# Performance work log

Measured on AMD Instinct MI355X. Metric: run time of the kernel, lower is better.

Reference implementation:

```python
import jax, jax.numpy as jnp
import numpy as np

B, IN, OUT, FAN = 2048, 4096, 4096, 64

def setup_inputs() -> dict:
    key = jax.random.key(0)
    k1, k2, k3, k4 = jax.random.split(key, 4)
    input = jax.random.normal(k1, (B, IN), dtype=jnp.float32)
    condensed_weight = jax.random.normal(k2, (OUT, FAN), dtype=jnp.float32) * 0.05
    bias = jax.random.normal(k3, (OUT,), dtype=jnp.float32) * 0.05
    input_mask = jax.random.randint(k4, (OUT, FAN), 0, IN, dtype=jnp.int64)
    return {"input": input, "condensed_weight": condensed_weight,
            "bias": bias, "input_mask": input_mask}

def reference(input, condensed_weight, bias, input_mask):
    # Per output neuron o: sum_f input[b, idx[o,f]] * w[o,f] + bias[o]
    # gathered: [B, OUT, FAN] -- the structured-sparse gather
    gathered = jnp.take(input, input_mask, axis=1)
    return jnp.einsum("bof,of->bo", gathered, condensed_weight) + bias
```

## Files before the change

### kernel.cpp

```cpp
#include <hip/hip_runtime.h>

#define B_DIM   2048
#define IN_DIM  4096
#define OUT_DIM 4096
#define FAN     64


typedef float v2f __attribute__((ext_vector_type(2)));

__device__ __forceinline__ unsigned bf16_rne(float f) {
    unsigned u = __float_as_uint(f);
    return (u + 0x7fffu + ((u >> 16) & 1u)) >> 16;
}

__global__ __launch_bounds__(256) void pack_kernel(
    const float* __restrict__ input, uint4* __restrict__ wsp)
{
    const int idx = blockIdx.x * 256 + threadIdx.x;
    const int t   = idx >> 11;
    const int c0  = (idx & 2047) << 1;

    const float* p = input + (size_t)t * 4 * IN_DIM + c0;
    const float2 r0 = *reinterpret_cast<const float2*>(p + 0 * IN_DIM);
    const float2 r1 = *reinterpret_cast<const float2*>(p + 1 * IN_DIM);
    const float2 r2 = *reinterpret_cast<const float2*>(p + 2 * IN_DIM);
    const float2 r3 = *reinterpret_cast<const float2*>(p + 3 * IN_DIM);

    uint4 q;
    q.x = bf16_rne(r0.x) | (bf16_rne(r1.x) << 16);
    q.y = bf16_rne(r2.x) | (bf16_rne(r3.x) << 16);
    q.z = bf16_rne(r0.y) | (bf16_rne(r1.y) << 16);
    q.w = bf16_rne(r2.y) | (bf16_rne(r3.y) << 16);

    wsp[(size_t)t * 2048 + (c0 >> 1)] = q;
}

__global__ __launch_bounds__(256, 2) void condensed_kernel(
    const uint4* __restrict__ wsp,
    const float* __restrict__ weight,
    const float* __restrict__ bias,
    const int*   __restrict__ mask,
    float*       __restrict__ out)
{
    __shared__ __align__(16) uint4 lds[2048];

    const int tid     = threadIdx.x;
    const int o       = blockIdx.y * 256 + tid;
    const int tbase   = blockIdx.x * 8;
    const int rowbase = blockIdx.x * 32;

    unsigned addrs[FAN];
    float    wv[FAN];
    {
        const int4*   mv = reinterpret_cast<const int4*>(mask)     + o * (FAN / 4);
        const float4* wp = reinterpret_cast<const float4*>(weight) + o * (FAN / 4);
        #pragma unroll
        for (int j = 0; j < FAN / 4; ++j) {
            int4   m4 = mv[j];
            float4 w4 = wp[j];
            addrs[4*j+0] = (unsigned)m4.x << 3;
            addrs[4*j+1] = (unsigned)m4.y << 3;
            addrs[4*j+2] = (unsigned)m4.z << 3;
            addrs[4*j+3] = (unsigned)m4.w << 3;
            wv[4*j+0] = w4.x;
            wv[4*j+1] = w4.y;
            wv[4*j+2] = w4.z;
            wv[4*j+3] = w4.w;
        }
    }
    const float bv = bias[o];

    const char* ldsb = reinterpret_cast<const char*>(lds);

    for (int t = 0; t < 8; ++t) {
        if (t) __syncthreads();

        {
            const uint4* src = wsp + (size_t)(tbase + t) * 2048 + tid;
            #pragma unroll
            for (int it = 0; it < 8; ++it) {
                __builtin_amdgcn_global_load_lds(
                    (const __attribute__((address_space(1))) unsigned*)(src + it * 256),
                    (__attribute__((address_space(3))) unsigned*)(lds + it * 256 + tid),
                    16, 0, 0);
            }
        }
        __syncthreads();

        {
            v2f a01 = {0.f, 0.f}, a23 = {0.f, 0.f};
            #pragma unroll
            for (int j = 0; j < FAN; ++j) {
                const uint2 g = *reinterpret_cast<const uint2*>(ldsb + addrs[j]);
                const v2f w2 = {wv[j], wv[j]};
                v2f v;
                v.x = __uint_as_float(g.x << 16);
                v.y = __uint_as_float(g.x & 0xffff0000u);
                a01 = __builtin_elementwise_fma(v, w2, a01);
                v.x = __uint_as_float(g.y << 16);
                v.y = __uint_as_float(g.y & 0xffff0000u);
                a23 = __builtin_elementwise_fma(v, w2, a23);
            }
            float* op = out + (size_t)(rowbase + 4 * t) * OUT_DIM + o;
            op[0 * OUT_DIM] = a01.x + bv;
            op[1 * OUT_DIM] = a01.y + bv;
            op[2 * OUT_DIM] = a23.x + bv;
            op[3 * OUT_DIM] = a23.y + bv;
        }
    }
}

extern "C" void kernel_launch(void* const* d_in, const int* in_sizes, int n_in,
                              void* d_out, int out_size, void* d_ws, size_t ws_size,
                              hipStream_t stream) {
    const float* input  = (const float*)d_in[0];
    const float* weight = (const float*)d_in[1];
    const float* bias   = (const float*)d_in[2];
    const int*   mask   = (const int*)d_in[3];
    float*       out    = (float*)d_out;
    uint4*       wsp    = (uint4*)d_ws;

    pack_kernel<<<4096, 256, 0, stream>>>(input, wsp);
    dim3 grid(64, 16);
    condensed_kernel<<<grid, 256, 0, stream>>>(wsp, weight, bias, mask, out);
}
```

Baseline: 134.7 us.

## Fuse bf16 pack into gather kernel with double-buffered LDS tiles

Drops the separate pack kernel. The gather kernel now loads fp32 input rows itself, converts them to bf16 in registers, and writes them into double-buffered LDS with a new swizzled layout. Blocks grow to 512 threads, with two threads per output neuron each taking half of an 8-row tile, over 128 rows per block, and the next tile's global loads overlap the current gather. This removes the workspace round trip and a launch, but leaves only 256 blocks at one block per CU, uses 128KB of LDS and much higher register pressure.

New measurement: 296.7 us. +120.3%, slower.

```diff
diff --git a/kernel.cpp b/kernel.cpp
--- a/kernel.cpp
+++ b/kernel.cpp
@@ -13,55 +13,87 @@
     return (u + 0x7fffu + ((u >> 16) & 1u)) >> 16;
 }
 
-__global__ __launch_bounds__(256) void pack_kernel(
-    const float* __restrict__ input, uint4* __restrict__ wsp)
-{
-    const int idx = blockIdx.x * 256 + threadIdx.x;
-    const int t   = idx >> 11;
-    const int c0  = (idx & 2047) << 1;
-
-    const float* p = input + (size_t)t * 4 * IN_DIM + c0;
-    const float2 r0 = *reinterpret_cast<const float2*>(p + 0 * IN_DIM);
-    const float2 r1 = *reinterpret_cast<const float2*>(p + 1 * IN_DIM);
-    const float2 r2 = *reinterpret_cast<const float2*>(p + 2 * IN_DIM);
-    const float2 r3 = *reinterpret_cast<const float2*>(p + 3 * IN_DIM);
-
-    uint4 q;
-    q.x = bf16_rne(r0.x) | (bf16_rne(r1.x) << 16);
-    q.y = bf16_rne(r2.x) | (bf16_rne(r3.x) << 16);
-    q.z = bf16_rne(r0.y) | (bf16_rne(r1.y) << 16);
-    q.w = bf16_rne(r2.y) | (bf16_rne(r3.y) << 16);
-
-    wsp[(size_t)t * 2048 + (c0 >> 1)] = q;
+__device__ __forceinline__ float f4e(const float4& v, int i) {
+    return reinterpret_cast<const float*>(&v)[i];
 }
 
-__global__ __launch_bounds__(256, 2) void condensed_kernel(
-    const uint4* __restrict__ wsp,
+#define LOADT(t)                                                              \
+    {                                                                         \
+        const float* s0 = input + (size_t)(rowbase + 8 * (t)) * IN_DIM + (tid << 2); \
+        _Pragma("unroll")                                                     \
+        for (int r = 0; r < 8; ++r) {                                         \
+            st[r]     = *reinterpret_cast<const float4*>(s0 + (size_t)r * IN_DIM);        \
+            st[8 + r] = *reinterpret_cast<const float4*>(s0 + (size_t)r * IN_DIM + 2048); \
+        }                                                                     \
+    }
+
+#define CWRITE(BUF)                                                           \
+    {                                                                         \
+        _Pragma("unroll")                                                     \
+        for (int k = 0; k < 2; ++k) {                                         \
+            _Pragma("unroll")                                                 \
+            for (int i = 0; i < 4; ++i) {                                     \
+                uint4 q;                                                      \
+                q.x = bf16_rne(f4e(st[8*k+0], i)) | (bf16_rne(f4e(st[8*k+1], i)) << 16); \
+                q.y = bf16_rne(f4e(st[8*k+2], i)) | (bf16_rne(f4e(st[8*k+3], i)) << 16); \
+                q.z = bf16_rne(f4e(st[8*k+4], i)) | (bf16_rne(f4e(st[8*k+5], i)) << 16); \
+                q.w = bf16_rne(f4e(st[8*k+6], i)) | (bf16_rne(f4e(st[8*k+7], i)) << 16); \
+                *reinterpret_cast<uint4*>(ldsw + (BUF) + k * 32768             \
+                    + ((tid >> 3) << 9) + (i << 7) + ((tid & 7) << 4)) = q;    \
+            }                                                                 \
+        }                                                                     \
+    }
+
+#define GATHER(BUF, t)                                                        \
+    {                                                                         \
+        v2f a01 = {0.f, 0.f}, a23 = {0.f, 0.f};                               \
+        _Pragma("unroll")                                                     \
+        for (int j = 0; j < FAN; ++j) {                                       \
+            const uint2 g = *reinterpret_cast<const uint2*>(ldsb + (BUF) + addrs[j]); \
+            const v2f w2 = {wv[j], wv[j]};                                    \
+            v2f v;                                                            \
+            v.x = __uint_as_float(g.x << 16);                                 \
+            v.y = __uint_as_float(g.x & 0xffff0000u);                         \
+            a01 = __builtin_elementwise_fma(v, w2, a01);                      \
+            v.x = __uint_as_float(g.y << 16);                                 \
+            v.y = __uint_as_float(g.y & 0xffff0000u);                         \
+            a23 = __builtin_elementwise_fma(v, w2, a23);                      \
+        }                                                                     \
+        float* op = out + (size_t)(rowbase + 8 * (t) + ((tid & 1) << 2)) * OUT_DIM + o; \
+        op[0 * OUT_DIM] = a01.x + bv;                                         \
+        op[1 * OUT_DIM] = a01.y + bv;                                         \
+        op[2 * OUT_DIM] = a23.x + bv;                                         \
+        op[3 * OUT_DIM] = a23.y + bv;                                         \
+    }
+
+__global__ __launch_bounds__(512, 1) void fused_kernel(
+    const float* __restrict__ input,
     const float* __restrict__ weight,
     const float* __restrict__ bias,
     const int*   __restrict__ mask,
     float*       __restrict__ out)
 {
-    __shared__ __align__(16) uint4 lds[2048];
+    __shared__ __align__(16) uint4 lds[8192];
 
     const int tid     = threadIdx.x;
-    const int o       = blockIdx.y * 256 + tid;
-    const int tbase   = blockIdx.x * 8;
-    const int rowbase = blockIdx.x * 32;
+    const int o       = blockIdx.y * 256 + (tid >> 1);
+    const int rowbase = blockIdx.x * 128;
 
     unsigned addrs[FAN];
     float    wv[FAN];
     {
         const int4*   mv = reinterpret_cast<const int4*>(mask)     + o * (FAN / 4);
         const float4* wp = reinterpret_cast<const float4*>(weight) + o * (FAN / 4);
+        const unsigned hoff = (unsigned)(tid & 1) << 3;
         #pragma unroll
         for (int j = 0; j < FAN / 4; ++j) {
             int4   m4 = mv[j];
             float4 w4 = wp[j];
-            addrs[4*j+0] = (unsigned)m4.x << 3;
-            addrs[4*j+1] = (unsigned)m4.y << 3;
-            addrs[4*j+2] = (unsigned)m4.z << 3;
-            addrs[4*j+3] = (unsigned)m4.w << 3;
+            int id;
+            id = m4.x; addrs[4*j+0] = (((unsigned)id >> 5) << 9) | (((unsigned)id & 3) << 7) | ((((unsigned)id >> 2) & 7) << 4) | hoff;
+            id = m4.y; addrs[4*j+1] = (((unsigned)id >> 5) << 9) | (((unsigned)id & 3) << 7) | ((((unsigned)id >> 2) & 7) << 4) | hoff;
+            id = m4.z; addrs[4*j+2] = (((unsigned)id >> 5) << 9) | (((unsigned)id & 3) << 7) | ((((unsigned)id >> 2) & 7) << 4) | hoff;
+            id = m4.w; addrs[4*j+3] = (((unsigned)id >> 5) << 9) | (((unsigned)id & 3) << 7) | ((((unsigned)id >> 2) & 7) << 4) | hoff;
             wv[4*j+0] = w4.x;
             wv[4*j+1] = w4.y;
             wv[4*j+2] = w4.z;
@@ -71,42 +103,27 @@
     const float bv = bias[o];
 
     const char* ldsb = reinterpret_cast<const char*>(lds);
+    char*       ldsw = reinterpret_cast<char*>(lds);
+    float4 st[16];
 
-    for (int t = 0; t < 8; ++t) {
-        if (t) __syncthreads();
+    LOADT(0);
+    CWRITE(0);
+    __syncthreads();
 
-        {
-            const uint4* src = wsp + (size_t)(tbase + t) * 2048 + tid;
-            #pragma unroll
-            for (int it = 0; it < 8; ++it) {
-                __builtin_amdgcn_global_load_lds(
-                    (const __attribute__((address_space(1))) unsigned*)(src + it * 256),
-                    (__attribute__((address_space(3))) unsigned*)(lds + it * 256 + tid),
-                    16, 0, 0);
-            }
+    for (int hp = 0; hp < 8; ++hp) {
+        LOADT(2 * hp + 1);
+        GATHER(0, 2 * hp);
+        CWRITE(65536);
+        __syncthreads();
+
+        if (hp < 7) {
+            LOADT(2 * hp + 2);
+            GATHER(65536, 2 * hp + 1);
+            CWRITE(0);
+        } else {
+            GATHER(65536, 2 * hp + 1);
         }
         __syncthreads();
-
-        {
-            v2f a01 = {0.f, 0.f}, a23 = {0.f, 0.f};
-            #pragma unroll
-            for (int j = 0; j < FAN; ++j) {
-                const uint2 g = *reinterpret_cast<const uint2*>(ldsb + addrs[j]);
-                const v2f w2 = {wv[j], wv[j]};
-                v2f v;
-                v.x = __uint_as_float(g.x << 16);
-                v.y = __uint_as_float(g.x & 0xffff0000u);
-                a01 = __builtin_elementwise_fma(v, w2, a01);
-                v.x = __uint_as_float(g.y << 16);
-                v.y = __uint_as_float(g.y & 0xffff0000u);
-                a23 = __builtin_elementwise_fma(v, w2, a23);
-            }
-            float* op = out + (size_t)(rowbase + 4 * t) * OUT_DIM + o;
-            op[0 * OUT_DIM] = a01.x + bv;
-            op[1 * OUT_DIM] = a01.y + bv;
-            op[2 * OUT_DIM] = a23.x + bv;
-            op[3 * OUT_DIM] = a23.y + bv;
-        }
     }
 }
 
@@ -118,9 +135,8 @@
     const float* bias   = (const float*)d_in[2];
     const int*   mask   = (const int*)d_in[3];
     float*       out    = (float*)d_out;
-    uint4*       wsp    = (uint4*)d_ws;
+    (void)d_ws; (void)ws_size;
 
-    pack_kernel<<<4096, 256, 0, stream>>>(input, wsp);
-    dim3 grid(64, 16);
-    condensed_kernel<<<grid, 256, 0, stream>>>(wsp, weight, bias, mask, out);
+    dim3 grid(16, 16);
+    fused_kernel<<<grid, 512, 0, stream>>>(input, weight, bias, mask, out);
 }
```
